# Optimization experiments

Hardware: AMD Instinct MI355X
Metric: run time of the kernel (lower is better)

## Reference

```python
import jax, jax.numpy as jnp
import numpy as np

B = 16384          # number of bags / MLP batch
L = 50             # indices per bag (uniform offsets)
N = B * L          # total indices
V = 10_000_000     # num_embeddings
D = 3              # embedding dim (fixed by EmbeddingBag(num_embeddings, 3))
K = 13             # MLP input width


def setup_inputs() -> dict:
    key = jax.random.key(0)
    ks = jax.random.split(key, 10)
    eb_input = jax.random.randint(ks[0], (N,), 0, V, dtype=jnp.int32)
    eb_offset = (jnp.arange(B, dtype=jnp.int32) * L)  # sorted, starts at 0
    mlp_input = jax.random.normal(ks[1], (B, K), dtype=jnp.float32)
    # single shared table: [EmbeddingBag]*3 in torch aliases one module
    emb_weight = jax.random.normal(ks[2], (V, D), dtype=jnp.float32) * 0.01
    w0 = jax.random.normal(ks[3], (12, K), dtype=jnp.float32) * (1.0 / np.sqrt(K))
    b0 = jax.random.normal(ks[4], (12,), dtype=jnp.float32) * 0.01
    w1 = jax.random.normal(ks[5], (6, 12), dtype=jnp.float32) * (1.0 / np.sqrt(12))
    b1 = jax.random.normal(ks[6], (6,), dtype=jnp.float32) * 0.01
    w2 = jax.random.normal(ks[7], (3, 6), dtype=jnp.float32) * (1.0 / np.sqrt(6))
    b2 = jax.random.normal(ks[8], (3,), dtype=jnp.float32) * 0.01
    return {"eb_input": eb_input, "eb_offset": eb_offset, "mlp_input": mlp_input,
            "emb_weight": emb_weight, "w0": w0, "b0": b0,
            "w1": w1, "b1": b1, "w2": w2, "b2": b2}


def _embedding_bag_mean(weight, indices, offsets, num_bags):
    # torch EmbeddingBag default mode='mean': per-bag mean of gathered rows
    n = indices.shape[0]
    # bag id for every index position (generic variable-offset handling)
    bag_ids = jnp.searchsorted(offsets, jnp.arange(n, dtype=offsets.dtype), side='right') - 1
    gathered = weight[indices]                                   # [N, D]
    sums = jax.ops.segment_sum(gathered, bag_ids, num_segments=num_bags)  # [B, D]
    counts = jnp.diff(jnp.append(offsets, n)).astype(weight.dtype)        # [B]
    return sums / counts[:, None]


def reference(eb_input, eb_offset, mlp_input, emb_weight, w0, b0, w1, b1, w2, b2):
    eb_out = _embedding_bag_mean(emb_weight, eb_input, eb_offset, B)  # [B, 3]
    # three EmbeddingBag calls share the same weight => identical outputs
    h = mlp_input @ w0.T + b0
    h = h @ w1.T + b1
    mlp_out = h @ w2.T + b2                                           # [B, 3]
    return jnp.concatenate([eb_out, eb_out, eb_out, mlp_out], axis=1)  # [B, 12]
```

## Files before the change

### kernel.cpp

```cpp
#include <hip/hip_runtime.h>

#define BAGS       16384
#define KIN        13
#define EB_BLOCKS  1024
#define MLP_BLOCKS 64

__global__ __launch_bounds__(256) void fused_kernel(
    const int* __restrict__ idxs, const int* __restrict__ offs,
    const float* __restrict__ W, const float* __restrict__ x,
    const float* __restrict__ w0, const float* __restrict__ b0,
    const float* __restrict__ w1, const float* __restrict__ b1,
    const float* __restrict__ w2, const float* __restrict__ b2,
    float* __restrict__ out, int n_total)
{
    if (blockIdx.x < EB_BLOCKS) {
        int tid = (int)(blockIdx.x * 256 + threadIdx.x);
        int bag = tid >> 4;
        int sl  = (int)(threadIdx.x & 15);

        int start = offs[bag];
        int end   = (bag + 1 < BAGS) ? offs[bag + 1] : n_total;
        int cnt   = end - start;

        float s0 = 0.f, s1 = 0.f, s2 = 0.f;

        if (cnt == 50) {
            int i0 = start + sl;
            int ia = idxs[i0];
            int ib = idxs[i0 + 16];
            int ic = idxs[i0 + 32];
            const float* ra = W + (size_t)ia * 3;
            const float* rb = W + (size_t)ib * 3;
            const float* rc = W + (size_t)ic * 3;
            float a0 = ra[0], a1 = ra[1], a2 = ra[2];
            float e0 = rb[0], e1 = rb[1], e2 = rb[2];
            float c0 = rc[0], c1 = rc[1], c2 = rc[2];
            s0 = a0 + e0 + c0;
            s1 = a1 + e1 + c1;
            s2 = a2 + e2 + c2;
            if (sl < 2) {
                int idd = idxs[i0 + 48];
                const float* rd = W + (size_t)idd * 3;
                s0 += rd[0]; s1 += rd[1]; s2 += rd[2];
            }
        } else {
            for (int i = start + sl; i < end; i += 16) {
                int idx = idxs[i];
                const float* r = W + (size_t)idx * 3;
                s0 += r[0]; s1 += r[1]; s2 += r[2];
            }
        }

        #pragma unroll
        for (int m = 8; m >= 1; m >>= 1) {
            s0 += __shfl_xor(s0, m, 16);
            s1 += __shfl_xor(s1, m, 16);
            s2 += __shfl_xor(s2, m, 16);
        }

        if (sl < 9) {
            float inv = 1.0f / (float)cnt;
            int c = sl % 3;
            float e = (c == 0 ? s0 : (c == 1 ? s1 : s2)) * inv;
            out[(size_t)bag * 12 + sl] = e;
        }
    } else {
        int b = (int)((blockIdx.x - EB_BLOCKS) * 256 + threadIdx.x);
        if (b >= BAGS) return;

        float xi[KIN];
        #pragma unroll
        for (int k = 0; k < KIN; ++k) xi[k] = x[(size_t)b * KIN + k];

        float h0[12];
        #pragma unroll
        for (int j = 0; j < 12; ++j) {
            float acc = b0[j];
            #pragma unroll
            for (int k = 0; k < KIN; ++k) acc += w0[j * KIN + k] * xi[k];
            h0[j] = acc;
        }

        float h1[6];
        #pragma unroll
        for (int j = 0; j < 6; ++j) {
            float acc = b1[j];
            #pragma unroll
            for (int k = 0; k < 12; ++k) acc += w1[j * 12 + k] * h0[k];
            h1[j] = acc;
        }

        float* o = out + (size_t)b * 12 + 9;
        #pragma unroll
        for (int j = 0; j < 3; ++j) {
            float acc = b2[j];
            #pragma unroll
            for (int k = 0; k < 6; ++k) acc += w2[j * 6 + k] * h1[k];
            o[j] = acc;
        }
    }
}

extern "C" void kernel_launch(void* const* d_in, const int* in_sizes, int n_in,
                              void* d_out, int out_size, void* d_ws, size_t ws_size,
                              hipStream_t stream) {
    const int*   eb_input   = (const int*)  d_in[0];
    const int*   eb_offset  = (const int*)  d_in[1];
    const float* mlp_input  = (const float*)d_in[2];
    const float* emb_weight = (const float*)d_in[3];
    const float* w0 = (const float*)d_in[4];
    const float* b0 = (const float*)d_in[5];
    const float* w1 = (const float*)d_in[6];
    const float* b1 = (const float*)d_in[7];
    const float* w2 = (const float*)d_in[8];
    const float* b2 = (const float*)d_in[9];
    float* out = (float*)d_out;

    int n_total = in_sizes[0];

    fused_kernel<<<EB_BLOCKS + MLP_BLOCKS, 256, 0, stream>>>(
        eb_input, eb_offset, emb_weight, mlp_input,
        w0, b0, w1, b1, w2, b2, out, n_total);
}
```

Baseline: 24.63 us.

## Bucket embedding lookups by row range before gathering to improve locality

Splits the fused kernel into three stages. The first bins every index into buckets of contiguous embedding rows through shared and global atomics. The second gathers the rows bucket by bucket into a position-ordered scratch buffer, and the third reduces the bags and runs the MLP. The aim is to make the random 12-byte table reads more local in cache. The cost is extra launches, a memset, atomics, scratch writes and reads, and a fixed per-bucket capacity that silently drops entries when it overflows.

Result: slower. 66.50 us (+170.0%).

```diff
diff --git a/kernel.cpp b/kernel.cpp
--- a/kernel.cpp
+++ b/kernel.cpp
@@ -1,63 +1,96 @@
 #include <hip/hip_runtime.h>
 
-#define BAGS       16384
-#define KIN        13
-#define EB_BLOCKS  1024
-#define MLP_BLOCKS 64
+#define KIN    13
+#define SHIFT  15
+#define CAP    3072
+#define BPB    12
+#define NBMAX  320
 
-__global__ __launch_bounds__(256) void fused_kernel(
-    const int* __restrict__ idxs, const int* __restrict__ offs,
-    const float* __restrict__ W, const float* __restrict__ x,
+
+__global__ __launch_bounds__(256) void k_bin(
+    const int* __restrict__ idxs, int* __restrict__ counters,
+    uint2* __restrict__ entries, int n_total, int NBK)
+{
+    __shared__ int scnt[NBMAX];
+    __shared__ int sbase[NBMAX];
+    int tid = (int)threadIdx.x;
+    for (int b = tid; b < NBK; b += 256) scnt[b] = 0;
+    __syncthreads();
+
+    int p0 = (int)blockIdx.x * 1280;
+    int bck[5], rank[5]; unsigned idxv[5]; bool ok[5];
+    #pragma unroll
+    for (int r = 0; r < 5; ++r) {
+        int i = p0 + r * 256 + tid;
+        ok[r] = (i < n_total);
+        bck[r] = 0; rank[r] = 0; idxv[r] = 0;
+        if (ok[r]) {
+            unsigned idx = (unsigned)__builtin_nontemporal_load(&idxs[i]);
+            idxv[r] = idx;
+            bck[r]  = (int)(idx >> SHIFT);
+            rank[r] = atomicAdd(&scnt[bck[r]], 1);
+        }
+    }
+    __syncthreads();
+    for (int b = tid; b < NBK; b += 256) {
+        int c = scnt[b];
+        sbase[b] = c ? atomicAdd(&counters[b], c) : 0;
+    }
+    __syncthreads();
+    #pragma unroll
+    for (int r = 0; r < 5; ++r) {
+        if (ok[r]) {
+            int slot = sbase[bck[r]] + rank[r];
+            if (slot < CAP)
+                entries[(size_t)bck[r] * CAP + slot] =
+                    make_uint2(idxv[r], (unsigned)(p0 + r * 256 + tid));
+        }
+    }
+}
+
+__global__ __launch_bounds__(256) void k_gather(
+    const uint2* __restrict__ entries, const int* __restrict__ counters,
+    const float* __restrict__ W, float* __restrict__ val)
+{
+    int bucket = (int)(blockIdx.x / BPB);
+    int slot   = (int)((blockIdx.x % BPB) * 256 + threadIdx.x);
+    if (slot >= counters[bucket]) return;
+
+    uint2 e = entries[(size_t)bucket * CAP + slot];
+    const float* r = W + (size_t)e.x * 3;
+    float v0 = r[0], v1 = r[1], v2 = r[2];
+    float* o = val + (size_t)e.y * 3;
+    o[0] = v0; o[1] = v1; o[2] = v2;
+}
+
+__global__ __launch_bounds__(256) void k_final(
+    const float* __restrict__ val, const int* __restrict__ offs,
+    const float* __restrict__ x,
     const float* __restrict__ w0, const float* __restrict__ b0,
     const float* __restrict__ w1, const float* __restrict__ b1,
     const float* __restrict__ w2, const float* __restrict__ b2,
-    float* __restrict__ out, int n_total)
+    float* __restrict__ out, int n_total, int B)
 {
-    if (blockIdx.x < EB_BLOCKS) {
-        int tid = (int)(blockIdx.x * 256 + threadIdx.x);
-        int bag = tid >> 4;
+    int ebBlocks = (B + 15) / 16;
+    if (blockIdx.x < (unsigned)ebBlocks) {
+        int bag = (int)(blockIdx.x * 16 + (threadIdx.x >> 4));
         int sl  = (int)(threadIdx.x & 15);
-
+        if (bag >= B) return;
         int start = offs[bag];
-        int end   = (bag + 1 < BAGS) ? offs[bag + 1] : n_total;
+        int end   = (bag + 1 < B) ? offs[bag + 1] : n_total;
         int cnt   = end - start;
 
         float s0 = 0.f, s1 = 0.f, s2 = 0.f;
-
-        if (cnt == 50) {
-            int i0 = start + sl;
-            int ia = idxs[i0];
-            int ib = idxs[i0 + 16];
-            int ic = idxs[i0 + 32];
-            const float* ra = W + (size_t)ia * 3;
-            const float* rb = W + (size_t)ib * 3;
-            const float* rc = W + (size_t)ic * 3;
-            float a0 = ra[0], a1 = ra[1], a2 = ra[2];
-            float e0 = rb[0], e1 = rb[1], e2 = rb[2];
-            float c0 = rc[0], c1 = rc[1], c2 = rc[2];
-            s0 = a0 + e0 + c0;
-            s1 = a1 + e1 + c1;
-            s2 = a2 + e2 + c2;
-            if (sl < 2) {
-                int idd = idxs[i0 + 48];
-                const float* rd = W + (size_t)idd * 3;
-                s0 += rd[0]; s1 += rd[1]; s2 += rd[2];
-            }
-        } else {
-            for (int i = start + sl; i < end; i += 16) {
-                int idx = idxs[i];
-                const float* r = W + (size_t)idx * 3;
-                s0 += r[0]; s1 += r[1]; s2 += r[2];
-            }
+        for (int i = start + sl; i < end; i += 16) {
+            const float* r = val + (size_t)i * 3;
+            s0 += r[0]; s1 += r[1]; s2 += r[2];
         }
-
         #pragma unroll
         for (int m = 8; m >= 1; m >>= 1) {
             s0 += __shfl_xor(s0, m, 16);
             s1 += __shfl_xor(s1, m, 16);
             s2 += __shfl_xor(s2, m, 16);
         }
-
         if (sl < 9) {
             float inv = 1.0f / (float)cnt;
             int c = sl % 3;
@@ -65,8 +98,8 @@
             out[(size_t)bag * 12 + sl] = e;
         }
     } else {
-        int b = (int)((blockIdx.x - EB_BLOCKS) * 256 + threadIdx.x);
-        if (b >= BAGS) return;
+        int b = (int)((blockIdx.x - ebBlocks) * 256 + threadIdx.x);
+        if (b >= B) return;
 
         float xi[KIN];
         #pragma unroll
@@ -80,7 +113,6 @@
             for (int k = 0; k < KIN; ++k) acc += w0[j * KIN + k] * xi[k];
             h0[j] = acc;
         }
-
         float h1[6];
         #pragma unroll
         for (int j = 0; j < 6; ++j) {
@@ -89,7 +121,6 @@
             for (int k = 0; k < 12; ++k) acc += w1[j * 12 + k] * h0[k];
             h1[j] = acc;
         }
-
         float* o = out + (size_t)b * 12 + 9;
         #pragma unroll
         for (int j = 0; j < 3; ++j) {
@@ -117,8 +148,26 @@
     float* out = (float*)d_out;
 
     int n_total = in_sizes[0];
+    int B       = in_sizes[1];
+    int V       = in_sizes[3] / 3;
+    int NBK     = (V + (1 << SHIFT) - 1) >> SHIFT;
+    if (NBK > NBMAX) NBK = NBMAX;
 
-    fused_kernel<<<EB_BLOCKS + MLP_BLOCKS, 256, 0, stream>>>(
-        eb_input, eb_offset, emb_weight, mlp_input,
-        w0, b0, w1, b1, w2, b2, out, n_total);
+    int*   counters = (int*)d_ws;
+    uint2* entries  = (uint2*)((char*)d_ws + 4096);
+    float* val      = (float*)((char*)d_ws + (8u << 20));
+
+    (void)hipMemsetAsync(counters, 0, (size_t)NBK * sizeof(int), stream);
+
+    int bin_blocks = (n_total + 1279) / 1280;
+    k_bin<<<bin_blocks, 256, 0, stream>>>(eb_input, counters, entries,
+                                          n_total, NBK);
+
+    k_gather<<<NBK * BPB, 256, 0, stream>>>(entries, counters, emb_weight, val);
+
+    int ebBlocks  = (B + 15) / 16;
+    int mlpBlocks = (B + 255) / 256;
+    k_final<<<ebBlocks + mlpBlocks, 256, 0, stream>>>(val, eb_offset, mlp_input,
+                                                      w0, b0, w1, b1, w2, b2,
+                                                      out, n_total, B);
 }
```
